# Performance work log

Hardware: AMD Instinct MI355X
Metric: run time of the kernel (lower is better)

Reference implementation:

```python
import jax, jax.numpy as jnp
import numpy as np

B, C, H, W = 8, 4, 64, 2048
KH, KW = 3, 5
PH, PW = KH // 2, KW // 2
NUM_ITERS = 3
THETA_GAMMA = 0.9
THETA_ALPHA = 0.9
THETA_BETA = 0.015


def smoothness_kernel(theta):
    # Gaussian over squared window offsets, center zeroed, placed on class diagonal
    hs = jnp.arange(KH, dtype=jnp.float32) - KH // 2
    ws = jnp.arange(KW, dtype=jnp.float32) - KW // 2
    pdist = hs[:, None] ** 2 + ws[None, :] ** 2  # (KH,KW)
    k = jnp.exp(-pdist / (2.0 * theta ** 2))
    k = k.at[KH // 2, KW // 2].set(0.0)
    kernel = jnp.zeros((C, C, KH, KW), jnp.float32)
    kernel = kernel.at[jnp.arange(C), jnp.arange(C)].set(k)
    return kernel


def unfold_neighbors(x):
    # x: (b, c, H, W) -> (b, c, KH*KW-1, H*W), center tap excluded; row-major (kh,kw)
    b, c = x.shape[0], x.shape[1]
    xp = jnp.pad(x, ((0, 0), (0, 0), (PH, PH), (PW, PW)))
    taps = [xp[:, :, dh:dh + H, dw:dw + W]
            for dh in range(KH) for dw in range(KW)]
    K = KH * KW
    del taps[K // 2]  # exclude center pixel
    patches = jnp.stack(taps, axis=2)  # (b, c, K-1, H, W)
    return patches.reshape(b, c, K - 1, H * W)


def conv_same(x, kernel):
    return jax.lax.conv_general_dilated(
        x, kernel, window_strides=(1, 1), padding=[(PH, PH), (PW, PW)],
        dimension_numbers=('NCHW', 'OIHW', 'NCHW'))


def setup_inputs() -> dict:
    key = jax.random.key(0)
    k1, k2, k3 = jax.random.split(key, 3)
    unary = jax.random.normal(k1, (B, C, H, W), jnp.float32)
    xyz = jax.random.normal(k2, (B, 3, H, W), jnp.float32)
    mask = (jax.random.uniform(k3, (B, H, W)) > 0.1).astype(jnp.float32)
    weight_appearance = jnp.ones((1, C, 1, 1), jnp.float32) * 0.1
    weight_smoothness = jnp.ones((1, C, 1, 1), jnp.float32) * 0.02
    compat_w = 1.0 - jnp.eye(C, dtype=jnp.float32)  # Potts label compatibility (O,I)
    return {
        'unary': unary, 'xyz': xyz, 'mask': mask,
        'weight_appearance': weight_appearance,
        'weight_smoothness': weight_smoothness,
        'compat_w': compat_w,
    }


def reference(unary, xyz, mask, weight_appearance, weight_smoothness, compat_w):
    kernel_gamma = smoothness_kernel(THETA_GAMMA)
    kernel_alpha = smoothness_kernel(THETA_ALPHA)
    theta_beta = jnp.full((C,), THETA_BETA, jnp.float32)

    # precompute appearance (bilateral) kernel from xyz; detached in the original
    anchor = xyz.reshape(B, 3, 1, H * W)
    nb = unfold_neighbors(xyz)  # (B,3,14,HW)
    pdist = ((nb - anchor) ** 2).sum(axis=1, keepdims=True)  # (B,1,14,HW)
    kernel_beta = jnp.exp(-pdist / (2.0 * theta_beta[None, :, None, None] ** 2))  # (B,C,14,HW)
    kernel_beta = jax.lax.stop_gradient(kernel_beta)

    m = mask[:, None]  # (B,1,H,W)
    Q = unary
    for _ in range(NUM_ITERS):
        Q = jax.nn.softmax(Q, axis=1)
        k_smooth = conv_same(Q, kernel_gamma)
        # appearance message passing: masked windowed gather weighted by kernel_beta
        masked_Q = Q * m
        Q_nb = unfold_neighbors(masked_Q)  # (B,C,14,HW)
        exp_app = (Q_nb * kernel_beta).sum(axis=2).reshape(B, C, H, W) * m
        exp_smooth = conv_same(Q, kernel_alpha)
        k_app = exp_app * exp_smooth
        weighted_k = weight_smoothness * k_smooth + weight_appearance * k_app
        pairwise = jnp.einsum('oc,bchw->bohw', compat_w, weighted_k)
        Q = unary - pairwise
    return Q
```

## Files before the change

kernel.cpp:

```cpp
#include <hip/hip_runtime.h>

#define Bsz 8
#define Cn  4
#define Hn  64
#define Wn  2048
#define HW  (Hn*Wn)

#define TW 64
#define TH 4
#define HALO_W (TW+4)
#define HALO_H (TH+2)
#define NHALO (HALO_W*HALO_H)

#define G1 0.53940824f
#define G2 0.29096127f
#define G4 0.08465836f
#define G5 0.04566536f

__global__ __launch_bounds__(256) void crf_iter(const float* __restrict__ Qin,
                                                const float* __restrict__ unary,
                                                const float* __restrict__ xyz,
                                                const float* __restrict__ mask,
                                                const float* __restrict__ wa,
                                                const float* __restrict__ wsm,
                                                const float* __restrict__ compat,
                                                float* __restrict__ Qout) {
    __shared__ float4 Sl[NHALO];
    __shared__ float4 Xl[NHALO];

    const int tid = threadIdx.x;
    const int w0 = blockIdx.x * TW;
    const int h0 = blockIdx.y * TH;
    const int b  = blockIdx.z;

    const size_t qbase = (size_t)b * Cn * HW;
    const size_t xbase = (size_t)b * 3 * HW;
    const size_t mbase = (size_t)b * HW;

    for (int i = tid; i < NHALO; i += 256) {
        int hr = i / HALO_W;
        int hw = i - hr * HALO_W;
        int gh = h0 + hr - 1;
        int gw = w0 + hw - 2;
        float4 s  = make_float4(0.f, 0.f, 0.f, 0.f);
        float4 xm = make_float4(0.f, 0.f, 0.f, 0.f);
        if (gh >= 0 && gh < Hn && gw >= 0 && gw < Wn) {
            size_t p = (size_t)gh * Wn + gw;
            float q0 = Qin[qbase + p];
            float q1 = Qin[qbase + p + HW];
            float q2 = Qin[qbase + p + 2 * HW];
            float q3 = Qin[qbase + p + 3 * HW];
            float mx = fmaxf(fmaxf(q0, q1), fmaxf(q2, q3));
            float e0 = __expf(q0 - mx), e1 = __expf(q1 - mx);
            float e2 = __expf(q2 - mx), e3 = __expf(q3 - mx);
            float inv = 1.0f / (e0 + e1 + e2 + e3);
            s = make_float4(e0 * inv, e1 * inv, e2 * inv, e3 * inv);
            xm = make_float4(xyz[xbase + p], xyz[xbase + p + HW],
                             xyz[xbase + p + 2 * HW], mask[mbase + p]);
        }
        Sl[i] = s;
        Xl[i] = xm;
    }
    __syncthreads();

    const int lw = (tid & 63) + 2;
    const int lr = (tid >> 6) + 1;
    const int gw = w0 + (tid & 63);
    const int gh = h0 + (tid >> 6);
    const size_t p = (size_t)gh * Wn + gw;

    const float4 xc = Xl[lr * HALO_W + lw];
    const float mc = xc.w;

    const float Gt[3][5] = {
        {G5, G2, G1, G2, G5},
        {G4, G1, 0.f, G1, G4},
        {G5, G2, G1, G2, G5}};

    float ksm0 = 0.f, ksm1 = 0.f, ksm2 = 0.f, ksm3 = 0.f;
    float app0 = 0.f, app1 = 0.f, app2 = 0.f, app3 = 0.f;

#pragma unroll
    for (int dh = -1; dh <= 1; ++dh) {
#pragma unroll
        for (int dw = -2; dw <= 2; ++dw) {
            if (dh == 0 && dw == 0) continue;
            const int li = (lr + dh) * HALO_W + (lw + dw);
            float4 s  = Sl[li];
            float4 xm = Xl[li];
            const float g = Gt[dh + 1][dw + 2];
            ksm0 += g * s.x; ksm1 += g * s.y; ksm2 += g * s.z; ksm3 += g * s.w;
            float dx = xm.x - xc.x;
            float dy = xm.y - xc.y;
            float dz = xm.z - xc.z;
            float beta = __expf(-2222.2222f * (dx * dx + dy * dy + dz * dz));
            float bm = beta * xm.w;
            app0 += bm * s.x; app1 += bm * s.y; app2 += bm * s.z; app3 += bm * s.w;
        }
    }

    float wk0 = ksm0 * (wsm[0] + wa[0] * (app0 * mc));
    float wk1 = ksm1 * (wsm[1] + wa[1] * (app1 * mc));
    float wk2 = ksm2 * (wsm[2] + wa[2] * (app2 * mc));
    float wk3 = ksm3 * (wsm[3] + wa[3] * (app3 * mc));

#pragma unroll
    for (int o = 0; o < Cn; ++o) {
        float pw = compat[o * 4 + 0] * wk0 + compat[o * 4 + 1] * wk1 +
                   compat[o * 4 + 2] * wk2 + compat[o * 4 + 3] * wk3;
        Qout[qbase + p + (size_t)o * HW] = unary[qbase + p + (size_t)o * HW] - pw;
    }
}

extern "C" void kernel_launch(void* const* d_in, const int* in_sizes, int n_in,
                              void* d_out, int out_size, void* d_ws, size_t ws_size,
                              hipStream_t stream) {
    const float* unary  = (const float*)d_in[0];
    const float* xyz    = (const float*)d_in[1];
    const float* mask   = (const float*)d_in[2];
    const float* wa     = (const float*)d_in[3];
    const float* wsm    = (const float*)d_in[4];
    const float* compat = (const float*)d_in[5];
    float* outp = (float*)d_out;

    float* Q1 = (float*)d_ws;
    float* Q2 = Q1 + (size_t)Bsz * Cn * HW;

    dim3 grid(Wn / TW, Hn / TH, Bsz), blk(256);

    crf_iter<<<grid, blk, 0, stream>>>(unary, unary, xyz, mask, wa, wsm, compat, Q1);
    crf_iter<<<grid, blk, 0, stream>>>(Q1,    unary, xyz, mask, wa, wsm, compat, Q2);
    crf_iter<<<grid, blk, 0, stream>>>(Q2,    unary, xyz, mask, wa, wsm, compat, outp);
}
```

Baseline: 133.7 us.

## Pack xyz/mask and intermediate Q as float4, process two rows per thread

Adds a pre-pass that packs xyz and mask into one interleaved float4 array, and stores the intermediate Q buffers interleaved as float4 so halo loads become single vector loads. Tile height doubles to 8 rows, and each thread now computes two output rows, reusing each loaded shared-memory row for both. This cuts halo overhead and shared-memory reads per output, at the cost of an extra pack kernel, more workspace and more registers per thread.

```diff
diff --git a/kernel.cpp b/kernel.cpp
--- a/kernel.cpp
+++ b/kernel.cpp
@@ -5,9 +5,10 @@
 #define Hn  64
 #define Wn  2048
 #define HW  (Hn*Wn)
+#define NPIX (Bsz*HW)
 
 #define TW 64
-#define TH 4
+#define TH 8
 #define HALO_W (TW+4)
 #define HALO_H (TH+2)
 #define NHALO (HALO_W*HALO_H)
@@ -17,14 +18,60 @@
 #define G4 0.08465836f
 #define G5 0.04566536f
 
-__global__ __launch_bounds__(256) void crf_iter(const float* __restrict__ Qin,
+__device__ __forceinline__ float4 f4fma(float a, const float4& v, const float4& acc) {
+    return make_float4(fmaf(a, v.x, acc.x), fmaf(a, v.y, acc.y),
+                       fmaf(a, v.z, acc.z), fmaf(a, v.w, acc.w));
+}
+
+__global__ __launch_bounds__(256) void pack_xm(const float* __restrict__ xyz,
+                                               const float* __restrict__ mask,
+                                               float4* __restrict__ XM) {
+    int t = blockIdx.x * 256 + threadIdx.x;
+    int p = t & (HW - 1);
+    int b = t >> 17;
+    size_t xb = (size_t)b * 3 * HW + p;
+    XM[t] = make_float4(xyz[xb], xyz[xb + HW], xyz[xb + 2 * HW],
+                        mask[(size_t)b * HW + p]);
+}
+
+template<bool OUT_PLANAR>
+__device__ __forceinline__ void epilogue(const float4& ksm, const float4& app, float mc,
+                                         const float* __restrict__ unary,
+                                         size_t qoff, size_t poff,
+                                         const float* __restrict__ wa,
+                                         const float* __restrict__ wsm,
+                                         const float* __restrict__ compat,
+                                         float* __restrict__ Op, float4* __restrict__ Oi) {
+    float wk[4] = { ksm.x * (wsm[0] + wa[0] * (app.x * mc)),
+                    ksm.y * (wsm[1] + wa[1] * (app.y * mc)),
+                    ksm.z * (wsm[2] + wa[2] * (app.z * mc)),
+                    ksm.w * (wsm[3] + wa[3] * (app.w * mc)) };
+    float pw[4];
+#pragma unroll
+    for (int o = 0; o < 4; ++o)
+        pw[o] = compat[o * 4 + 0] * wk[0] + compat[o * 4 + 1] * wk[1] +
+                compat[o * 4 + 2] * wk[2] + compat[o * 4 + 3] * wk[3];
+    if (OUT_PLANAR) {
+#pragma unroll
+        for (int o = 0; o < 4; ++o)
+            Op[qoff + (size_t)o * HW] = unary[qoff + (size_t)o * HW] - pw[o];
+    } else {
+        float4 u = make_float4(unary[qoff], unary[qoff + HW],
+                               unary[qoff + 2 * HW], unary[qoff + 3 * HW]);
+        Oi[poff] = make_float4(u.x - pw[0], u.y - pw[1], u.z - pw[2], u.w - pw[3]);
+    }
+}
+
+template<bool IN_PLANAR, bool OUT_PLANAR>
+__global__ __launch_bounds__(256) void crf_iter(const float* __restrict__ Qp,
+                                                const float4* __restrict__ Qi,
                                                 const float* __restrict__ unary,
-                                                const float* __restrict__ xyz,
-                                                const float* __restrict__ mask,
+                                                const float4* __restrict__ XM,
                                                 const float* __restrict__ wa,
                                                 const float* __restrict__ wsm,
                                                 const float* __restrict__ compat,
-                                                float* __restrict__ Qout) {
+                                                float* __restrict__ Op,
+                                                float4* __restrict__ Oi) {
     __shared__ float4 Sl[NHALO];
     __shared__ float4 Xl[NHALO];
 
@@ -34,81 +81,98 @@
     const int b  = blockIdx.z;
 
     const size_t qbase = (size_t)b * Cn * HW;
-    const size_t xbase = (size_t)b * 3 * HW;
-    const size_t mbase = (size_t)b * HW;
-
-    for (int i = tid; i < NHALO; i += 256) {
-        int hr = i / HALO_W;
-        int hw = i - hr * HALO_W;
-        int gh = h0 + hr - 1;
-        int gw = w0 + hw - 2;
-        float4 s  = make_float4(0.f, 0.f, 0.f, 0.f);
-        float4 xm = make_float4(0.f, 0.f, 0.f, 0.f);
-        if (gh >= 0 && gh < Hn && gw >= 0 && gw < Wn) {
-            size_t p = (size_t)gh * Wn + gw;
-            float q0 = Qin[qbase + p];
-            float q1 = Qin[qbase + p + HW];
-            float q2 = Qin[qbase + p + 2 * HW];
-            float q3 = Qin[qbase + p + 3 * HW];
-            float mx = fmaxf(fmaxf(q0, q1), fmaxf(q2, q3));
-            float e0 = __expf(q0 - mx), e1 = __expf(q1 - mx);
-            float e2 = __expf(q2 - mx), e3 = __expf(q3 - mx);
-            float inv = 1.0f / (e0 + e1 + e2 + e3);
-            s = make_float4(e0 * inv, e1 * inv, e2 * inv, e3 * inv);
-            xm = make_float4(xyz[xbase + p], xyz[xbase + p + HW],
-                             xyz[xbase + p + 2 * HW], mask[mbase + p]);
+    const size_t pbase = (size_t)b * HW;
+
+#pragma unroll
+    for (int k = 0; k < 3; ++k) {
+        int i = tid + k * 256;
+        if (i < NHALO) {
+            int hr = i / HALO_W;
+            int hc = i - hr * HALO_W;
+            int gh = h0 + hr - 1;
+            int gw = w0 + hc - 2;
+            float4 s  = make_float4(0.f, 0.f, 0.f, 0.f);
+            float4 xm = make_float4(0.f, 0.f, 0.f, 0.f);
+            if (gh >= 0 && gh < Hn && gw >= 0 && gw < Wn) {
+                size_t p = (size_t)gh * Wn + gw;
+                float q0, q1, q2, q3;
+                if (IN_PLANAR) {
+                    q0 = Qp[qbase + p];
+                    q1 = Qp[qbase + p + HW];
+                    q2 = Qp[qbase + p + 2 * HW];
+                    q3 = Qp[qbase + p + 3 * HW];
+                } else {
+                    float4 q = Qi[pbase + p];
+                    q0 = q.x; q1 = q.y; q2 = q.z; q3 = q.w;
+                }
+                float mx = fmaxf(fmaxf(q0, q1), fmaxf(q2, q3));
+                float e0 = __expf(q0 - mx), e1 = __expf(q1 - mx);
+                float e2 = __expf(q2 - mx), e3 = __expf(q3 - mx);
+                float inv = 1.0f / (e0 + e1 + e2 + e3);
+                s  = make_float4(e0 * inv, e1 * inv, e2 * inv, e3 * inv);
+                xm = XM[pbase + p];
+            }
+            Sl[i] = s;
+            Xl[i] = xm;
         }
-        Sl[i] = s;
-        Xl[i] = xm;
     }
     __syncthreads();
 
-    const int lw = (tid & 63) + 2;
-    const int lr = (tid >> 6) + 1;
-    const int gw = w0 + (tid & 63);
-    const int gh = h0 + (tid >> 6);
-    const size_t p = (size_t)gh * Wn + gw;
-
-    const float4 xc = Xl[lr * HALO_W + lw];
-    const float mc = xc.w;
+    const int lane = tid & 63;
+    const int tr = tid >> 6;
+    const int r0 = 2 * tr;
+    const int lw = lane + 2;
+
+    const float4 xc0 = Xl[(r0 + 1) * HALO_W + lw];
+    const float4 xc1 = Xl[(r0 + 2) * HALO_W + lw];
+
+    float4 ksm0 = make_float4(0,0,0,0), app0 = make_float4(0,0,0,0);
+    float4 ksm1 = make_float4(0,0,0,0), app1 = make_float4(0,0,0,0);
 
     const float Gt[3][5] = {
         {G5, G2, G1, G2, G5},
         {G4, G1, 0.f, G1, G4},
         {G5, G2, G1, G2, G5}};
 
-    float ksm0 = 0.f, ksm1 = 0.f, ksm2 = 0.f, ksm3 = 0.f;
-    float app0 = 0.f, app1 = 0.f, app2 = 0.f, app3 = 0.f;
-
-#pragma unroll
-    for (int dh = -1; dh <= 1; ++dh) {
-#pragma unroll
-        for (int dw = -2; dw <= 2; ++dw) {
-            if (dh == 0 && dw == 0) continue;
-            const int li = (lr + dh) * HALO_W + (lw + dw);
-            float4 s  = Sl[li];
-            float4 xm = Xl[li];
-            const float g = Gt[dh + 1][dw + 2];
-            ksm0 += g * s.x; ksm1 += g * s.y; ksm2 += g * s.z; ksm3 += g * s.w;
-            float dx = xm.x - xc.x;
-            float dy = xm.y - xc.y;
-            float dz = xm.z - xc.z;
-            float beta = __expf(-2222.2222f * (dx * dx + dy * dy + dz * dz));
-            float bm = beta * xm.w;
-            app0 += bm * s.x; app1 += bm * s.y; app2 += bm * s.z; app3 += bm * s.w;
+#pragma unroll
+    for (int j = 0; j < 4; ++j) {
+        const int rbase = (r0 + j) * HALO_W + lw;
+        float4 s[5], x[5];
+#pragma unroll
+        for (int d = 0; d < 5; ++d) {
+            s[d] = Sl[rbase + d - 2];
+            x[d] = Xl[rbase + d - 2];
         }
-    }
-
-    float wk0 = ksm0 * (wsm[0] + wa[0] * (app0 * mc));
-    float wk1 = ksm1 * (wsm[1] + wa[1] * (app1 * mc));
-    float wk2 = ksm2 * (wsm[2] + wa[2] * (app2 * mc));
-    float wk3 = ksm3 * (wsm[3] + wa[3] * (app3 * mc));
-
-#pragma unroll
-    for (int o = 0; o < Cn; ++o) {
-        float pw = compat[o * 4 + 0] * wk0 + compat[o * 4 + 1] * wk1 +
-                   compat[o * 4 + 2] * wk2 + compat[o * 4 + 3] * wk3;
-        Qout[qbase + p + (size_t)o * HW] = unary[qbase + p + (size_t)o * HW] - pw;
+#pragma unroll
+        for (int d = 0; d < 5; ++d) {
+            if (j <= 2 && !(j == 1 && d == 2)) {
+                const float g = Gt[j][d];
+                ksm0 = f4fma(g, s[d], ksm0);
+                float dx = x[d].x - xc0.x, dy = x[d].y - xc0.y, dz = x[d].z - xc0.z;
+                float bm = __expf(-2222.2222f * (dx*dx + dy*dy + dz*dz)) * x[d].w;
+                app0 = f4fma(bm, s[d], app0);
+            }
+            if (j >= 1 && !(j == 2 && d == 2)) {
+                const float g = Gt[j - 1][d];
+                ksm1 = f4fma(g, s[d], ksm1);
+                float dx = x[d].x - xc1.x, dy = x[d].y - xc1.y, dz = x[d].z - xc1.z;
+                float bm = __expf(-2222.2222f * (dx*dx + dy*dy + dz*dz)) * x[d].w;
+                app1 = f4fma(bm, s[d], app1);
+            }
+        }
+    }
+
+    const int gw = w0 + lane;
+    const int gh0 = h0 + r0;
+    {
+        size_t p = (size_t)gh0 * Wn + gw;
+        epilogue<OUT_PLANAR>(ksm0, app0, xc0.w, unary, qbase + p, pbase + p,
+                             wa, wsm, compat, Op, Oi);
+    }
+    {
+        size_t p = (size_t)(gh0 + 1) * Wn + gw;
+        epilogue<OUT_PLANAR>(ksm1, app1, xc1.w, unary, qbase + p, pbase + p,
+                             wa, wsm, compat, Op, Oi);
     }
 }
 
@@ -123,12 +187,18 @@
     const float* compat = (const float*)d_in[5];
     float* outp = (float*)d_out;
 
-    float* Q1 = (float*)d_ws;
-    float* Q2 = Q1 + (size_t)Bsz * Cn * HW;
+    float4* XM = (float4*)d_ws;
+    float4* Q1 = XM + (size_t)NPIX;
+    float4* Q2 = Q1 + (size_t)NPIX;
 
     dim3 grid(Wn / TW, Hn / TH, Bsz), blk(256);
 
-    crf_iter<<<grid, blk, 0, stream>>>(unary, unary, xyz, mask, wa, wsm, compat, Q1);
-    crf_iter<<<grid, blk, 0, stream>>>(Q1,    unary, xyz, mask, wa, wsm, compat, Q2);
-    crf_iter<<<grid, blk, 0, stream>>>(Q2,    unary, xyz, mask, wa, wsm, compat, outp);
-}
+    pack_xm<<<dim3(NPIX / 256), blk, 0, stream>>>(xyz, mask, XM);
+
+    crf_iter<true, false><<<grid, blk, 0, stream>>>(unary, nullptr, unary, XM,
+                                                    wa, wsm, compat, nullptr, Q1);
+    crf_iter<false, false><<<grid, blk, 0, stream>>>(nullptr, Q1, unary, XM,
+                                                     wa, wsm, compat, nullptr, Q2);
+    crf_iter<false, true><<<grid, blk, 0, stream>>>(nullptr, Q2, unary, XM,
+                                                    wa, wsm, compat, outp, nullptr);
+}
```

Result: no change. 135.6 us (+1.4%).

## Fuse three CRF iterations into one kernel with overlapping halo recompute

Applied to the files above, without the earlier changes.

Replaces three separate kernel launches with a single kernel. Each block loads a tile with a 3-row by 6-column halo, then runs all three mean-field iterations out of shared memory, shrinking the computed region each time and ping-ponging between two softmax buffers. Each thread now computes two vertically adjacent pixels so that neighbor loads are shared between them. This removes the global round-trips of the intermediate Q arrays and two launches, at the cost of redundant halo computation (a 76x14 load region for a 64x8 output) and more shared memory per block, which may limit occupancy.

```diff
diff --git a/kernel.cpp b/kernel.cpp
--- a/kernel.cpp
+++ b/kernel.cpp
@@ -7,26 +7,130 @@
 #define HW  (Hn*Wn)
 
 #define TW 64
-#define TH 4
-#define HALO_W (TW+4)
-#define HALO_H (TH+2)
-#define NHALO (HALO_W*HALO_H)
+#define TH 8
+#define BW 76
+#define BH 14
+#define NB (BW*BH)
 
 #define G1 0.53940824f
 #define G2 0.29096127f
 #define G4 0.08465836f
 #define G5 0.04566536f
 
-__global__ __launch_bounds__(256) void crf_iter(const float* __restrict__ Qin,
-                                                const float* __restrict__ unary,
-                                                const float* __restrict__ xyz,
-                                                const float* __restrict__ mask,
-                                                const float* __restrict__ wa,
-                                                const float* __restrict__ wsm,
-                                                const float* __restrict__ compat,
-                                                float* __restrict__ Qout) {
-    __shared__ float4 Sl[NHALO];
-    __shared__ float4 Xl[NHALO];
+__device__ __forceinline__ float4 f4fma(float a, const float4& v, const float4& acc) {
+    return make_float4(fmaf(a, v.x, acc.x), fmaf(a, v.y, acc.y),
+                       fmaf(a, v.z, acc.z), fmaf(a, v.w, acc.w));
+}
+
+template<bool FINAL>
+__device__ __forceinline__ void finish_px(int gh, int gw, int bidx,
+                                          const float4& ksm, const float4& app, float mc,
+                                          const float* __restrict__ unary,
+                                          float* __restrict__ outp,
+                                          float4* __restrict__ Sout, size_t qbase,
+                                          const float* wa, const float* wsm,
+                                          const float* cw) {
+    bool inimg = (gh >= 0) & (gh < Hn) & (gw >= 0) & (gw < Wn);
+    if (inimg) {
+        size_t p = (size_t)gh * Wn + gw;
+        float wk0 = ksm.x * (wsm[0] + wa[0] * (app.x * mc));
+        float wk1 = ksm.y * (wsm[1] + wa[1] * (app.y * mc));
+        float wk2 = ksm.z * (wsm[2] + wa[2] * (app.z * mc));
+        float wk3 = ksm.w * (wsm[3] + wa[3] * (app.w * mc));
+        float q[4];
+#pragma unroll
+        for (int o = 0; o < 4; ++o) {
+            float pw = cw[o * 4 + 0] * wk0 + cw[o * 4 + 1] * wk1 +
+                       cw[o * 4 + 2] * wk2 + cw[o * 4 + 3] * wk3;
+            q[o] = unary[qbase + p + (size_t)o * HW] - pw;
+        }
+        if (FINAL) {
+#pragma unroll
+            for (int o = 0; o < 4; ++o)
+                outp[qbase + p + (size_t)o * HW] = q[o];
+        } else {
+            float mx = fmaxf(fmaxf(q[0], q[1]), fmaxf(q[2], q[3]));
+            float e0 = __expf(q[0] - mx), e1 = __expf(q[1] - mx);
+            float e2 = __expf(q[2] - mx), e3 = __expf(q[3] - mx);
+            float inv = 1.0f / (e0 + e1 + e2 + e3);
+            Sout[bidx] = make_float4(e0 * inv, e1 * inv, e2 * inv, e3 * inv);
+        }
+    } else if (!FINAL) {
+        Sout[bidx] = make_float4(0.f, 0.f, 0.f, 0.f);
+    }
+}
+
+template<int RW, int RH, int OY, int OX, bool FINAL>
+__device__ __forceinline__ void do_iter(const float4* __restrict__ Sin,
+                                        float4* __restrict__ Sout,
+                                        const float4* __restrict__ X,
+                                        const float* __restrict__ unary,
+                                        float* __restrict__ outp,
+                                        size_t qbase, int h0, int w0, int tid,
+                                        const float* wa, const float* wsm,
+                                        const float* cw) {
+    const float Gt[3][5] = {
+        {G5, G2, G1, G2, G5},
+        {G4, G1, 0.f, G1, G4},
+        {G5, G2, G1, G2, G5}};
+    constexpr int P = RW * (RH / 2);
+    for (int i = tid; i < P; i += 256) {
+        int pr = i / RW;
+        int pc = i - pr * RW;
+        int r0 = OY + 2 * pr;
+        int c  = OX + pc;
+        int b0 = (r0 + 3) * BW + (c + 6);
+
+        float4 xc0 = X[b0];
+        float4 xc1 = X[b0 + BW];
+        float4 ksm0 = make_float4(0,0,0,0), app0 = make_float4(0,0,0,0);
+        float4 ksm1 = make_float4(0,0,0,0), app1 = make_float4(0,0,0,0);
+
+#pragma unroll
+        for (int j = 0; j < 4; ++j) {
+            int rb = b0 + (j - 1) * BW;
+            float4 s[5], x[5];
+#pragma unroll
+            for (int d = 0; d < 5; ++d) {
+                s[d] = Sin[rb + d - 2];
+                x[d] = X[rb + d - 2];
+            }
+#pragma unroll
+            for (int d = 0; d < 5; ++d) {
+                if (j <= 2 && !(j == 1 && d == 2)) {
+                    ksm0 = f4fma(Gt[j][d], s[d], ksm0);
+                    float dx = x[d].x - xc0.x, dy = x[d].y - xc0.y, dz = x[d].z - xc0.z;
+                    float bm = __expf(-2222.2222f * (dx*dx + dy*dy + dz*dz)) * x[d].w;
+                    app0 = f4fma(bm, s[d], app0);
+                }
+                if (j >= 1 && !(j == 2 && d == 2)) {
+                    ksm1 = f4fma(Gt[j - 1][d], s[d], ksm1);
+                    float dx = x[d].x - xc1.x, dy = x[d].y - xc1.y, dz = x[d].z - xc1.z;
+                    float bm = __expf(-2222.2222f * (dx*dx + dy*dy + dz*dz)) * x[d].w;
+                    app1 = f4fma(bm, s[d], app1);
+                }
+            }
+        }
+
+        int gw = w0 + c;
+        int gh0 = h0 + r0;
+        finish_px<FINAL>(gh0,     gw, b0,      ksm0, app0, xc0.w, unary, outp, Sout,
+                         qbase, wa, wsm, cw);
+        finish_px<FINAL>(gh0 + 1, gw, b0 + BW, ksm1, app1, xc1.w, unary, outp, Sout,
+                         qbase, wa, wsm, cw);
+    }
+}
+
+__global__ __launch_bounds__(256, 3) void crf_fused(const float* __restrict__ unary,
+                                                    const float* __restrict__ xyz,
+                                                    const float* __restrict__ mask,
+                                                    const float* __restrict__ wa_g,
+                                                    const float* __restrict__ wsm_g,
+                                                    const float* __restrict__ cw_g,
+                                                    float* __restrict__ outp) {
+    __shared__ float4 SA[NB];
+    __shared__ float4 SB[NB];
+    __shared__ float4 X[NB];
 
     const int tid = threadIdx.x;
     const int w0 = blockIdx.x * TW;
@@ -37,19 +141,25 @@
     const size_t xbase = (size_t)b * 3 * HW;
     const size_t mbase = (size_t)b * HW;
 
-    for (int i = tid; i < NHALO; i += 256) {
-        int hr = i / HALO_W;
-        int hw = i - hr * HALO_W;
-        int gh = h0 + hr - 1;
-        int gw = w0 + hw - 2;
+    float wa[4], wsm[4], cw[16];
+#pragma unroll
+    for (int k = 0; k < 4; ++k) { wa[k] = wa_g[k]; wsm[k] = wsm_g[k]; }
+#pragma unroll
+    for (int k = 0; k < 16; ++k) cw[k] = cw_g[k];
+
+    for (int i = tid; i < NB; i += 256) {
+        int br = i / BW;
+        int bc = i - br * BW;
+        int gh = h0 + br - 3;
+        int gw = w0 + bc - 6;
         float4 s  = make_float4(0.f, 0.f, 0.f, 0.f);
         float4 xm = make_float4(0.f, 0.f, 0.f, 0.f);
         if (gh >= 0 && gh < Hn && gw >= 0 && gw < Wn) {
             size_t p = (size_t)gh * Wn + gw;
-            float q0 = Qin[qbase + p];
-            float q1 = Qin[qbase + p + HW];
-            float q2 = Qin[qbase + p + 2 * HW];
-            float q3 = Qin[qbase + p + 3 * HW];
+            float q0 = unary[qbase + p];
+            float q1 = unary[qbase + p + HW];
+            float q2 = unary[qbase + p + 2 * HW];
+            float q3 = unary[qbase + p + 3 * HW];
             float mx = fmaxf(fmaxf(q0, q1), fmaxf(q2, q3));
             float e0 = __expf(q0 - mx), e1 = __expf(q1 - mx);
             float e2 = __expf(q2 - mx), e3 = __expf(q3 - mx);
@@ -58,58 +168,16 @@
             xm = make_float4(xyz[xbase + p], xyz[xbase + p + HW],
                              xyz[xbase + p + 2 * HW], mask[mbase + p]);
         }
-        Sl[i] = s;
-        Xl[i] = xm;
+        SA[i] = s;
+        X[i] = xm;
     }
     __syncthreads();
 
-    const int lw = (tid & 63) + 2;
-    const int lr = (tid >> 6) + 1;
-    const int gw = w0 + (tid & 63);
-    const int gh = h0 + (tid >> 6);
-    const size_t p = (size_t)gh * Wn + gw;
-
-    const float4 xc = Xl[lr * HALO_W + lw];
-    const float mc = xc.w;
-
-    const float Gt[3][5] = {
-        {G5, G2, G1, G2, G5},
-        {G4, G1, 0.f, G1, G4},
-        {G5, G2, G1, G2, G5}};
-
-    float ksm0 = 0.f, ksm1 = 0.f, ksm2 = 0.f, ksm3 = 0.f;
-    float app0 = 0.f, app1 = 0.f, app2 = 0.f, app3 = 0.f;
-
-#pragma unroll
-    for (int dh = -1; dh <= 1; ++dh) {
-#pragma unroll
-        for (int dw = -2; dw <= 2; ++dw) {
-            if (dh == 0 && dw == 0) continue;
-            const int li = (lr + dh) * HALO_W + (lw + dw);
-            float4 s  = Sl[li];
-            float4 xm = Xl[li];
-            const float g = Gt[dh + 1][dw + 2];
-            ksm0 += g * s.x; ksm1 += g * s.y; ksm2 += g * s.z; ksm3 += g * s.w;
-            float dx = xm.x - xc.x;
-            float dy = xm.y - xc.y;
-            float dz = xm.z - xc.z;
-            float beta = __expf(-2222.2222f * (dx * dx + dy * dy + dz * dz));
-            float bm = beta * xm.w;
-            app0 += bm * s.x; app1 += bm * s.y; app2 += bm * s.z; app3 += bm * s.w;
-        }
-    }
-
-    float wk0 = ksm0 * (wsm[0] + wa[0] * (app0 * mc));
-    float wk1 = ksm1 * (wsm[1] + wa[1] * (app1 * mc));
-    float wk2 = ksm2 * (wsm[2] + wa[2] * (app2 * mc));
-    float wk3 = ksm3 * (wsm[3] + wa[3] * (app3 * mc));
-
-#pragma unroll
-    for (int o = 0; o < Cn; ++o) {
-        float pw = compat[o * 4 + 0] * wk0 + compat[o * 4 + 1] * wk1 +
-                   compat[o * 4 + 2] * wk2 + compat[o * 4 + 3] * wk3;
-        Qout[qbase + p + (size_t)o * HW] = unary[qbase + p + (size_t)o * HW] - pw;
-    }
+    do_iter<72, 12, -2, -4, false>(SA, SB, X, unary, nullptr, qbase, h0, w0, tid, wa, wsm, cw);
+    __syncthreads();
+    do_iter<68, 10, -1, -2, false>(SB, SA, X, unary, nullptr, qbase, h0, w0, tid, wa, wsm, cw);
+    __syncthreads();
+    do_iter<64,  8,  0,  0, true >(SA, nullptr, X, unary, outp, qbase, h0, w0, tid, wa, wsm, cw);
 }
 
 extern "C" void kernel_launch(void* const* d_in, const int* in_sizes, int n_in,
@@ -123,12 +191,6 @@
     const float* compat = (const float*)d_in[5];
     float* outp = (float*)d_out;
 
-    float* Q1 = (float*)d_ws;
-    float* Q2 = Q1 + (size_t)Bsz * Cn * HW;
-
     dim3 grid(Wn / TW, Hn / TH, Bsz), blk(256);
-
-    crf_iter<<<grid, blk, 0, stream>>>(unary, unary, xyz, mask, wa, wsm, compat, Q1);
-    crf_iter<<<grid, blk, 0, stream>>>(Q1,    unary, xyz, mask, wa, wsm, compat, Q2);
-    crf_iter<<<grid, blk, 0, stream>>>(Q2,    unary, xyz, mask, wa, wsm, compat, outp);
+    crf_fused<<<grid, blk, 0, stream>>>(unary, xyz, mask, wa, wsm, compat, outp);
 }
```

Result: slower. 138.9 us (+3.9%).
